# Performance work log

Hardware: AMD Instinct MI355X
Metric: run time of the kernel (lower is better)

The kernel has to match this reference:

```python
import jax, jax.numpy as jnp
import numpy as np

NODE_W, EDGE_W, HEADS = 512, 32, 8
DOT = NODE_W // HEADS
CLIP_MIN, CLIP_MAX = -5.0, 5.0
B, N = 4, 1024


def setup_inputs() -> dict:
    key = jax.random.key(0)
    ks = jax.random.split(key, 12)
    s = 0.02
    return {
        "nodes": jax.random.normal(ks[0], (B, N, NODE_W), dtype=jnp.float32),
        "edges": jax.random.normal(ks[1], (B, N, N, EDGE_W), dtype=jnp.float32),
        "Wq": jax.random.normal(ks[2], (NODE_W, NODE_W), dtype=jnp.float32) * s,
        "bq": jnp.zeros((NODE_W,), dtype=jnp.float32),
        "Wk": jax.random.normal(ks[3], (NODE_W, NODE_W), dtype=jnp.float32) * s,
        "bk": jnp.zeros((NODE_W,), dtype=jnp.float32),
        "Wv": jax.random.normal(ks[4], (NODE_W, NODE_W), dtype=jnp.float32) * s,
        "bv": jnp.zeros((NODE_W,), dtype=jnp.float32),
        "Wg": jax.random.normal(ks[5], (EDGE_W, HEADS), dtype=jnp.float32) * s,
        "bg": jnp.zeros((HEADS,), dtype=jnp.float32),
        "We": jax.random.normal(ks[6], (EDGE_W, HEADS), dtype=jnp.float32) * s,
        "be": jnp.zeros((HEADS,), dtype=jnp.float32),
    }


def reference(nodes, edges, Wq, bq, Wk, bk, Wv, bv, Wg, bg, We, be):
    b, n, _ = nodes.shape
    # projections, reshaped to [B, N, dot_dim, heads] as in the torch .view
    q = (nodes @ Wq + bq).reshape(b, n, DOT, HEADS)
    k = (nodes @ Wk + bk).reshape(b, n, DOT, HEADS)
    v = (nodes @ Wv + bv).reshape(b, n, DOT, HEADS)
    # raw scores [B, L, M, heads], scaled and clipped
    H = jnp.einsum('bldh,bmdh->blmh', q, k) / (DOT ** 0.5)
    H = jnp.clip(H, CLIP_MIN, CLIP_MAX)
    # edge bias and gate, each [B, N, N, heads]
    e = edges @ We + be
    g = edges @ Wg + bg
    H = H + e
    # softmax over key axis (dim=2), sigmoid gate multiply
    A = jax.nn.sigmoid(g) * jax.nn.softmax(H, axis=2)
    # dropout is identity in eval/deterministic mode
    attn = jnp.einsum('blmh,bmdh->bldh', A, v).reshape(b, n, NODE_W)
    return attn, H
```

## Files before the change

### kernel.cpp

```cpp
#include <hip/hip_runtime.h>
#include <hip/hip_bf16.h>
#include <stdint.h>

typedef float  f32x4  __attribute__((ext_vector_type(4)));
typedef short  bf16x8 __attribute__((ext_vector_type(8)));
typedef short  bf16x4 __attribute__((ext_vector_type(4)));

#define MFMA16(A,B,C) __builtin_amdgcn_mfma_f32_16x16x32_bf16(A,B,C,0,0,0)

__device__ __forceinline__ short f2bf(float x){
    union { float f; uint32_t u; } v; v.f = x;
    uint32_t r = v.u + 0x7fffu + ((v.u >> 16) & 1u);
    return (short)(r >> 16);
}
__device__ __forceinline__ float bf2f(short x){
    union { uint32_t u; float f; } v; v.u = ((uint32_t)(uint16_t)x) << 16;
    return v.f;
}
__device__ __forceinline__ bf16x8 pack8(f32x4 a, f32x4 b){
    bf16x8 r;
    r[0]=f2bf(a[0]); r[1]=f2bf(a[1]); r[2]=f2bf(a[2]); r[3]=f2bf(a[3]);
    r[4]=f2bf(b[0]); r[5]=f2bf(b[1]); r[6]=f2bf(b[2]); r[7]=f2bf(b[3]);
    return r;
}

__global__ void k_prep_wt(const float* __restrict__ Wq, const float* __restrict__ Wk,
                          const float* __restrict__ Wv, short* __restrict__ WT){
    int blk = blockIdx.x;
    int w  = blk >> 6;
    int t  = blk & 63;
    int k0 = (t >> 3) << 6;
    int o0 = (t & 7) << 6;
    const float* W = (w == 0) ? Wq : ((w == 1) ? Wk : Wv);
    __shared__ float tile[64][65];
    int tx = threadIdx.x & 63, ty = threadIdx.x >> 6;
    #pragma unroll
    for (int i = 0; i < 64; i += 4)
        tile[ty + i][tx] = W[(size_t)(k0 + ty + i) * 512 + o0 + tx];
    __syncthreads();
    short* out = WT + (size_t)w * 512 * 512;
    #pragma unroll
    for (int i = 0; i < 64; i += 4)
        out[(size_t)(o0 + ty + i) * 512 + k0 + tx] = f2bf(tile[tx][ty + i]);
}

__global__ void k_prep_wcat(const float* __restrict__ We, const float* __restrict__ Wg,
                            const float* __restrict__ be, const float* __restrict__ bg,
                            short* __restrict__ WcatT, float* __restrict__ bcat){
    int t = threadIdx.x;
    int ch = t >> 5, c = t & 31;
    float v = (ch < 8) ? We[c * 8 + ch] : Wg[c * 8 + (ch - 8)];
    WcatT[ch * 32 + c] = f2bf(v);
    if (t < 16) bcat[t] = (t < 8) ? be[t] : bg[t - 8];
}

__global__ void k_prep_nodes(const float* __restrict__ nodes, short* __restrict__ nb){
    size_t i = ((size_t)blockIdx.x * 256 + threadIdx.x) * 8;
    f32x4 a = *(const f32x4*)(nodes + i);
    f32x4 b = *(const f32x4*)(nodes + i + 4);
    *(bf16x8*)(nb + i) = pack8(a, b);
}

__global__ void k_qkv(const short* __restrict__ nodesbf, const short* __restrict__ WT,
                      const float* __restrict__ bq, const float* __restrict__ bk,
                      const float* __restrict__ bv,
                      short* __restrict__ qb, short* __restrict__ kb, short* __restrict__ vTb){
    int bx = blockIdx.x;
    int lt = bx & 255;
    int ob = bx >> 8;
    int wave = threadIdx.x >> 6, lane = threadIdx.x & 63;
    int lr = lane & 15, lg = lane >> 4;
    int row0 = lt << 4;
    int og = ob * 256 + wave * 64;
    int w  = og >> 9;
    int oo = og & 511;

    const short* Wp = WT + (size_t)w * 512 * 512;
    f32x4 acc[4] = {};
    const short* arow = nodesbf + (size_t)(row0 + lr) * 512 + lg * 8;
    #pragma unroll
    for (int kk = 0; kk < 16; ++kk){
        bf16x8 af = *(const bf16x8*)(arow + kk * 32);
        #pragma unroll
        for (int s = 0; s < 4; ++s){
            const short* bp = Wp + (size_t)(oo + s * 16 + lr) * 512 + kk * 32 + lg * 8;
            bf16x8 bfv = *(const bf16x8*)bp;
            acc[s] = MFMA16(af, bfv, acc[s]);
        }
    }
    const float* bias = (w == 0) ? bq : ((w == 1) ? bk : bv);
    int b  = row0 >> 10;
    int lb = (row0 & 1023) + lg * 4;
    #pragma unroll
    for (int s = 0; s < 4; ++s){
        int o = oo + s * 16 + lr;
        float bsv = bias[o];
        int h = o & 7, d = o >> 3;
        #pragma unroll
        for (int r = 0; r < 4; ++r){
            float v = acc[s][r] + bsv;
            short sv = f2bf(v);
            int l = lb + r;
            if (w == 0)       qb [((size_t)(b * 8 + h) * 1024 + l) * 64 + d] = sv;
            else if (w == 1)  kb [((size_t)(b * 8 + h) * 1024 + l) * 64 + d] = sv;
            else              vTb[((size_t)(b * 8 + h) * 64 + d) * 1024 + l] = sv;
        }
    }
}

__global__ void k_hsg(const float* __restrict__ edges, const short* __restrict__ qb,
                      const short* __restrict__ kb, const short* __restrict__ WcatT,
                      const float* __restrict__ bcat,
                      float* __restrict__ Hout, short* __restrict__ Pb,
                      float* __restrict__ psum){
    int bx = blockIdx.x;
    int mt = bx & 15;
    int lt = (bx >> 4) & 63;
    int b  = bx >> 10;
    int wave = threadIdx.x >> 6, lane = threadIdx.x & 63;
    int lr = lane & 15, lg = lane >> 4;
    int l0 = lt << 4;
    int m0 = mt * 64 + wave * 16;

    __shared__ short eg[4][16][16][24];

    f32x4 S[8] = {};
    #pragma unroll
    for (int h = 0; h < 8; ++h){
        #pragma unroll
        for (int half = 0; half < 2; ++half){
            bf16x8 qf = *(const bf16x8*)(qb + ((size_t)(b * 8 + h) * 1024 + l0 + lr) * 64 + half * 32 + lg * 8);
            bf16x8 kf = *(const bf16x8*)(kb + ((size_t)(b * 8 + h) * 1024 + m0 + lr) * 64 + half * 32 + lg * 8);
            S[h] = MFMA16(qf, kf, S[h]);
        }
    }

    bf16x8 wf = *(const bf16x8*)(WcatT + lr * 32 + lg * 8);
    f32x4 bc = *(const f32x4*)(bcat + lg * 4);
    f32x4 zero = {0.f, 0.f, 0.f, 0.f};
    #pragma unroll
    for (int l = 0; l < 16; ++l){
        const float* ep = edges + ((size_t)(b * 1024 + l0 + l) * 1024 + m0 + lr) * 32 + lg * 8;
        f32x4 e0 = *(const f32x4*)ep;
        f32x4 e1 = *(const f32x4*)(ep + 4);
        bf16x8 ef = pack8(e0, e1);
        f32x4 d = MFMA16(wf, ef, zero);
        bf16x4 dv;
        #pragma unroll
        for (int r = 0; r < 4; ++r) dv[r] = f2bf(d[r] + bc[r]);
        *(bf16x4*)&eg[wave][l][lr][lg * 4] = dv;
    }

    #pragma unroll
    for (int r = 0; r < 4; ++r){
        int l = lg * 4 + r;
        bf16x8 e8 = *(const bf16x8*)&eg[wave][l][lr][0];
        bf16x8 g8 = *(const bf16x8*)&eg[wave][l][lr][8];
        float Hv[8], ex[8], sg[8];
        #pragma unroll
        for (int h = 0; h < 8; ++h){
            float s = S[h][r] * 0.125f;
            s = fminf(fmaxf(s, -5.f), 5.f);
            Hv[h] = s + bf2f(e8[h]);
            ex[h] = __expf(Hv[h]);
            sg[h] = __builtin_amdgcn_rcpf(1.f + __expf(-bf2f(g8[h])));
        }
        size_t idx = ((size_t)(b * 1024 + l0 + l) * 1024 + m0 + lr) * 8;
        f32x4 h0 = {Hv[0], Hv[1], Hv[2], Hv[3]};
        f32x4 h1 = {Hv[4], Hv[5], Hv[6], Hv[7]};
        *(f32x4*)(Hout + idx)     = h0;
        *(f32x4*)(Hout + idx + 4) = h1;
        #pragma unroll
        for (int h = 0; h < 8; ++h){
            Pb[((size_t)(b * 8 + h) * 1024 + l0 + l) * 1024 + m0 + lr] = f2bf(ex[h] * sg[h]);
            float t = ex[h];
            t += __shfl_xor(t, 1);
            t += __shfl_xor(t, 2);
            t += __shfl_xor(t, 4);
            t += __shfl_xor(t, 8);
            if (lr == 0)
                psum[((size_t)(b * 8 + h) * 1024 + l0 + l) * 64 + mt * 4 + wave] = t;
        }
    }
}

__global__ void k_pv(const short* __restrict__ Pb, const float* __restrict__ psum,
                     const short* __restrict__ vTb, float* __restrict__ attn){
    int b  = blockIdx.x >> 6;
    int lt = blockIdx.x & 63;
    int h    = threadIdx.x >> 6;
    int lane = threadIdx.x & 63;
    int lr = lane & 15, lg = lane >> 4;
    int l0 = lt << 4;

    const short* Prow  = Pb  + ((size_t)(b * 8 + h) * 1024 + l0 + lr) * 1024 + lg * 8;
    const short* vbase = vTb + (size_t)(b * 8 + h) * 64 * 1024 + (size_t)lr * 1024 + lg * 8;

    f32x4 O[4] = {};
    for (int m0 = 0; m0 < 1024; m0 += 32){
        bf16x8 pf = *(const bf16x8*)(Prow + m0);
        #pragma unroll
        for (int dt = 0; dt < 4; ++dt){
            bf16x8 vf = *(const bf16x8*)(vbase + (size_t)dt * 16 * 1024 + m0);
            O[dt] = MFMA16(vf, pf, O[dt]);
        }
    }

    const float* pp = psum + ((size_t)(b * 8 + h) * 1024 + l0 + lr) * 64 + lg * 16;
    f32x4 s0 = *(const f32x4*)pp;
    f32x4 s1 = *(const f32x4*)(pp + 4);
    f32x4 s2 = *(const f32x4*)(pp + 8);
    f32x4 s3 = *(const f32x4*)(pp + 12);
    float ds = (s0[0]+s0[1]+s0[2]+s0[3]) + (s1[0]+s1[1]+s1[2]+s1[3])
             + (s2[0]+s2[1]+s2[2]+s2[3]) + (s3[0]+s3[1]+s3[2]+s3[3]);
    ds += __shfl_xor(ds, 16);
    ds += __shfl_xor(ds, 32);
    float inv = __builtin_amdgcn_rcpf(ds);

    __shared__ float Os[16][516];
    #pragma unroll
    for (int dt = 0; dt < 4; ++dt){
        #pragma unroll
        for (int r = 0; r < 4; ++r)
            Os[lr][(dt * 16 + lg * 4 + r) * 8 + h] = O[dt][r] * inv;
    }
    __syncthreads();
    int row = threadIdx.x >> 5;
    int cb  = (threadIdx.x & 31) * 16;
    float* dst = attn + ((size_t)(b * 1024 + l0 + row)) * 512 + cb;
    #pragma unroll
    for (int j = 0; j < 16; j += 4)
        *(f32x4*)(dst + j) = *(const f32x4*)&Os[row][cb + j];
}

#define OFF_WT    ((size_t)0x0000000)
#define OFF_WCAT  ((size_t)0x0180000)
#define OFF_BCAT  ((size_t)0x0180400)
#define OFF_NB    ((size_t)0x0200000)
#define OFF_Q     ((size_t)0x0600000)
#define OFF_K     ((size_t)0x0A00000)
#define OFF_VT    ((size_t)0x0E00000)
#define OFF_P     ((size_t)0x1200000)
#define OFF_PS    ((size_t)0x5200000)

extern "C" void kernel_launch(void* const* d_in, const int* in_sizes, int n_in,
                              void* d_out, int out_size, void* d_ws, size_t ws_size,
                              hipStream_t stream) {
    const float* nodes = (const float*)d_in[0];
    const float* edges = (const float*)d_in[1];
    const float* Wq = (const float*)d_in[2];
    const float* bq = (const float*)d_in[3];
    const float* Wk = (const float*)d_in[4];
    const float* bk = (const float*)d_in[5];
    const float* Wv = (const float*)d_in[6];
    const float* bv = (const float*)d_in[7];
    const float* Wg = (const float*)d_in[8];
    const float* bg = (const float*)d_in[9];
    const float* We = (const float*)d_in[10];
    const float* be = (const float*)d_in[11];

    float* out_attn = (float*)d_out;
    float* out_H    = out_attn + (size_t)4 * 1024 * 512;

    char* ws = (char*)d_ws;
    short* WT    = (short*)(ws + OFF_WT);
    short* WcatT = (short*)(ws + OFF_WCAT);
    float* bcat  = (float*)(ws + OFF_BCAT);
    short* nb    = (short*)(ws + OFF_NB);
    short* qb    = (short*)(ws + OFF_Q);
    short* kb    = (short*)(ws + OFF_K);
    short* vTb   = (short*)(ws + OFF_VT);
    short* Pb    = (short*)(ws + OFF_P);
    float* psum  = (float*)(ws + OFF_PS);

    k_prep_wt   <<<192, 256, 0, stream>>>(Wq, Wk, Wv, WT);
    k_prep_wcat <<<1, 512, 0, stream>>>(We, Wg, be, bg, WcatT, bcat);
    k_prep_nodes<<<1024, 256, 0, stream>>>(nodes, nb);
    k_qkv       <<<1536, 256, 0, stream>>>(nb, WT, bq, bk, bv, qb, kb, vTb);
    k_hsg       <<<4096, 256, 0, stream>>>(edges, qb, kb, WcatT, bcat, out_H, Pb, psum);
    k_pv        <<<256, 512, 0, stream>>>(Pb, psum, vTb, out_attn);
}
```

Before: 336.4 us.

## Fuse score/gate and PV kernels, keep probabilities in shared memory

Merges the score/edge-projection kernel and the P·V kernel into one kernel. Each block now owns 16 query rows and loops over all 1024 keys in chunks of 128. The gated probabilities are stored in a swizzled, double-buffered LDS tile and consumed right away by MFMA against V. The softmax denominators are accumulated in registers and reduced through LDS. This removes the global write and re-read of the bf16 P matrix and the partial-sum array, and edge loads are prefetched one step ahead in registers. In exchange the grid shrinks to 256 blocks of 512 threads with heavy register and LDS use, which lowers occupancy for an edges-bandwidth-bound stream.

After: 337.8 us. About the same (+0.4%).

```diff
diff --git a/kernel.cpp b/kernel.cpp
--- a/kernel.cpp
+++ b/kernel.cpp
@@ -108,129 +108,148 @@
     }
 }
 
-__global__ void k_hsg(const float* __restrict__ edges, const short* __restrict__ qb,
-                      const short* __restrict__ kb, const short* __restrict__ WcatT,
-                      const float* __restrict__ bcat,
-                      float* __restrict__ Hout, short* __restrict__ Pb,
-                      float* __restrict__ psum){
-    int bx = blockIdx.x;
-    int mt = bx & 15;
-    int lt = (bx >> 4) & 63;
-    int b  = bx >> 10;
-    int wave = threadIdx.x >> 6, lane = threadIdx.x & 63;
+__global__ __launch_bounds__(512, 2) void k_main(
+        const float* __restrict__ edges, const short* __restrict__ qb,
+        const short* __restrict__ kb, const short* __restrict__ vTb,
+        const short* __restrict__ WcatT, const float* __restrict__ bcat,
+        float* __restrict__ Hout, float* __restrict__ attn){
+    int hw = blockIdx.x;
+    int j  = hw & 7, kk0 = hw >> 3;
+    int b  = j >> 1;
+    int lt = ((j & 1) << 5) | kk0;
+    int l0 = lt << 4;
+
+    int w    = threadIdx.x >> 6;
+    int lane = threadIdx.x & 63;
     int lr = lane & 15, lg = lane >> 4;
-    int l0 = lt << 4;
-    int m0 = mt * 64 + wave * 16;
-
-    __shared__ short eg[4][16][16][24];
-
-    f32x4 S[8] = {};
+
+    __shared__ short eg[8][4][16][20];
+    __shared__ short Plds[2][8 * 16 * 128];
+    __shared__ float den[8][8][16];
+    __shared__ float Os[16][516];
+
+    bf16x8 wf = *(const bf16x8*)(WcatT + lr * 32 + lg * 8);
+    f32x4  bc = *(const f32x4*)(bcat + lg * 4);
+    const size_t bl0 = (size_t)(b * 1024 + l0);
+
+    f32x4 O[4] = {};
+    float dsum[8][4] = {};
+    f32x4 zero = {0.f, 0.f, 0.f, 0.f};
+
+    for (int iter = 0; iter < 8; ++iter){
+        const int m0 = iter * 128 + w * 16;
+        f32x4 S[8] = {};
+        #pragma unroll
+        for (int h = 0; h < 8; ++h){
+            #pragma unroll
+            for (int half = 0; half < 2; ++half){
+                bf16x8 qf = *(const bf16x8*)(qb + ((size_t)(b * 8 + h) * 1024 + l0 + lr) * 64 + half * 32 + lg * 8);
+                bf16x8 kf = *(const bf16x8*)(kb + ((size_t)(b * 8 + h) * 1024 + m0 + lr) * 64 + half * 32 + lg * 8);
+                S[h] = MFMA16(qf, kf, S[h]);
+            }
+        }
+
+        f32x4 ebuf[2][8];
+        #pragma unroll
+        for (int s = 0; s < 4; ++s){
+            const float* ep = edges + ((bl0 + 4 * s) * 1024 + m0 + lr) * 32 + lg * 8;
+            ebuf[0][2 * s]     = *(const f32x4*)ep;
+            ebuf[0][2 * s + 1] = *(const f32x4*)(ep + 4);
+        }
+        short* Pcur = &Plds[iter & 1][0];
+        #pragma unroll
+        for (int r = 0; r < 4; ++r){
+            if (r < 3){
+                #pragma unroll
+                for (int s = 0; s < 4; ++s){
+                    const float* ep = edges + ((bl0 + 4 * s + r + 1) * 1024 + m0 + lr) * 32 + lg * 8;
+                    ebuf[(r + 1) & 1][2 * s]     = *(const f32x4*)ep;
+                    ebuf[(r + 1) & 1][2 * s + 1] = *(const f32x4*)(ep + 4);
+                }
+            }
+            #pragma unroll
+            for (int s = 0; s < 4; ++s){
+                f32x4 d = MFMA16(wf, pack8(ebuf[r & 1][2 * s], ebuf[r & 1][2 * s + 1]), zero);
+                bf16x4 dv;
+                #pragma unroll
+                for (int rr = 0; rr < 4; ++rr) dv[rr] = f2bf(d[rr] + bc[rr]);
+                *(bf16x4*)&eg[w][s][lr][lg * 4] = dv;
+            }
+            int l = 4 * lg + r;
+            bf16x8 e8 = *(const bf16x8*)&eg[w][lg][lr][0];
+            bf16x8 g8 = *(const bf16x8*)&eg[w][lg][lr][8];
+            float Hv[8]; short pv[8];
+            #pragma unroll
+            for (int h = 0; h < 8; ++h){
+                float s = S[h][r] * 0.125f;
+                s = fminf(fmaxf(s, -5.f), 5.f);
+                float hv = s + bf2f(e8[h]);
+                Hv[h] = hv;
+                float ex = __expf(hv);
+                dsum[h][r] += ex;
+                float sg = __builtin_amdgcn_rcpf(1.f + __expf(-bf2f(g8[h])));
+                pv[h] = f2bf(ex * sg);
+            }
+            size_t idx = ((bl0 + l) * 1024 + m0 + lr) * 8;
+            f32x4 h0 = {Hv[0], Hv[1], Hv[2], Hv[3]};
+            f32x4 h1 = {Hv[4], Hv[5], Hv[6], Hv[7]};
+            *(f32x4*)(Hout + idx)     = h0;
+            *(f32x4*)(Hout + idx + 4) = h1;
+            #pragma unroll
+            for (int h = 0; h < 8; ++h){
+                int byte = ((h * 16 + l) << 8) + ((w * 16 + lr) << 1);
+                *(short*)((char*)Pcur + (byte ^ ((l & 7) << 4))) = pv[h];
+            }
+        }
+        __syncthreads();
+
+        const short* vbase = vTb + (size_t)(b * 8 + w) * 64 * 1024 + iter * 128;
+        #pragma unroll
+        for (int ks = 0; ks < 4; ++ks){
+            int mm = ks * 32 + lg * 8;
+            int byte = ((w * 16 + lr) << 8) + (mm << 1);
+            bf16x8 pf = *(const bf16x8*)((char*)Pcur + (byte ^ ((lr & 7) << 4)));
+            #pragma unroll
+            for (int dt = 0; dt < 4; ++dt){
+                bf16x8 vf = *(const bf16x8*)(vbase + (size_t)(dt * 16 + lr) * 1024 + mm);
+                O[dt] = MFMA16(vf, pf, O[dt]);
+            }
+        }
+    }
+
     #pragma unroll
     for (int h = 0; h < 8; ++h){
         #pragma unroll
-        for (int half = 0; half < 2; ++half){
-            bf16x8 qf = *(const bf16x8*)(qb + ((size_t)(b * 8 + h) * 1024 + l0 + lr) * 64 + half * 32 + lg * 8);
-            bf16x8 kf = *(const bf16x8*)(kb + ((size_t)(b * 8 + h) * 1024 + m0 + lr) * 64 + half * 32 + lg * 8);
-            S[h] = MFMA16(qf, kf, S[h]);
-        }
-    }
-
-    bf16x8 wf = *(const bf16x8*)(WcatT + lr * 32 + lg * 8);
-    f32x4 bc = *(const f32x4*)(bcat + lg * 4);
-    f32x4 zero = {0.f, 0.f, 0.f, 0.f};
-    #pragma unroll
-    for (int l = 0; l < 16; ++l){
-        const float* ep = edges + ((size_t)(b * 1024 + l0 + l) * 1024 + m0 + lr) * 32 + lg * 8;
-        f32x4 e0 = *(const f32x4*)ep;
-        f32x4 e1 = *(const f32x4*)(ep + 4);
-        bf16x8 ef = pack8(e0, e1);
-        f32x4 d = MFMA16(wf, ef, zero);
-        bf16x4 dv;
-        #pragma unroll
-        for (int r = 0; r < 4; ++r) dv[r] = f2bf(d[r] + bc[r]);
-        *(bf16x4*)&eg[wave][l][lr][lg * 4] = dv;
-    }
-
-    #pragma unroll
-    for (int r = 0; r < 4; ++r){
-        int l = lg * 4 + r;
-        bf16x8 e8 = *(const bf16x8*)&eg[wave][l][lr][0];
-        bf16x8 g8 = *(const bf16x8*)&eg[wave][l][lr][8];
-        float Hv[8], ex[8], sg[8];
-        #pragma unroll
-        for (int h = 0; h < 8; ++h){
-            float s = S[h][r] * 0.125f;
-            s = fminf(fmaxf(s, -5.f), 5.f);
-            Hv[h] = s + bf2f(e8[h]);
-            ex[h] = __expf(Hv[h]);
-            sg[h] = __builtin_amdgcn_rcpf(1.f + __expf(-bf2f(g8[h])));
-        }
-        size_t idx = ((size_t)(b * 1024 + l0 + l) * 1024 + m0 + lr) * 8;
-        f32x4 h0 = {Hv[0], Hv[1], Hv[2], Hv[3]};
-        f32x4 h1 = {Hv[4], Hv[5], Hv[6], Hv[7]};
-        *(f32x4*)(Hout + idx)     = h0;
-        *(f32x4*)(Hout + idx + 4) = h1;
-        #pragma unroll
-        for (int h = 0; h < 8; ++h){
-            Pb[((size_t)(b * 8 + h) * 1024 + l0 + l) * 1024 + m0 + lr] = f2bf(ex[h] * sg[h]);
-            float t = ex[h];
+        for (int r = 0; r < 4; ++r){
+            float t = dsum[h][r];
             t += __shfl_xor(t, 1);
             t += __shfl_xor(t, 2);
             t += __shfl_xor(t, 4);
             t += __shfl_xor(t, 8);
-            if (lr == 0)
-                psum[((size_t)(b * 8 + h) * 1024 + l0 + l) * 64 + mt * 4 + wave] = t;
-        }
-    }
-}
-
-__global__ void k_pv(const short* __restrict__ Pb, const float* __restrict__ psum,
-                     const short* __restrict__ vTb, float* __restrict__ attn){
-    int b  = blockIdx.x >> 6;
-    int lt = blockIdx.x & 63;
-    int h    = threadIdx.x >> 6;
-    int lane = threadIdx.x & 63;
-    int lr = lane & 15, lg = lane >> 4;
-    int l0 = lt << 4;
-
-    const short* Prow  = Pb  + ((size_t)(b * 8 + h) * 1024 + l0 + lr) * 1024 + lg * 8;
-    const short* vbase = vTb + (size_t)(b * 8 + h) * 64 * 1024 + (size_t)lr * 1024 + lg * 8;
-
-    f32x4 O[4] = {};
-    for (int m0 = 0; m0 < 1024; m0 += 32){
-        bf16x8 pf = *(const bf16x8*)(Prow + m0);
-        #pragma unroll
-        for (int dt = 0; dt < 4; ++dt){
-            bf16x8 vf = *(const bf16x8*)(vbase + (size_t)dt * 16 * 1024 + m0);
-            O[dt] = MFMA16(vf, pf, O[dt]);
-        }
-    }
-
-    const float* pp = psum + ((size_t)(b * 8 + h) * 1024 + l0 + lr) * 64 + lg * 16;
-    f32x4 s0 = *(const f32x4*)pp;
-    f32x4 s1 = *(const f32x4*)(pp + 4);
-    f32x4 s2 = *(const f32x4*)(pp + 8);
-    f32x4 s3 = *(const f32x4*)(pp + 12);
-    float ds = (s0[0]+s0[1]+s0[2]+s0[3]) + (s1[0]+s1[1]+s1[2]+s1[3])
-             + (s2[0]+s2[1]+s2[2]+s2[3]) + (s3[0]+s3[1]+s3[2]+s3[3]);
-    ds += __shfl_xor(ds, 16);
-    ds += __shfl_xor(ds, 32);
+            if (lr == 0) den[w][h][4 * lg + r] = t;
+        }
+    }
+    __syncthreads();
+    float ds = 0.f;
+    #pragma unroll
+    for (int w2 = 0; w2 < 8; ++w2) ds += den[w2][w][lr];
     float inv = __builtin_amdgcn_rcpf(ds);
 
-    __shared__ float Os[16][516];
     #pragma unroll
     for (int dt = 0; dt < 4; ++dt){
         #pragma unroll
         for (int r = 0; r < 4; ++r)
-            Os[lr][(dt * 16 + lg * 4 + r) * 8 + h] = O[dt][r] * inv;
+            Os[lr][(dt * 16 + 4 * lg + r) * 8 + w] = O[dt][r] * inv;
     }
     __syncthreads();
-    int row = threadIdx.x >> 5;
-    int cb  = (threadIdx.x & 31) * 16;
-    float* dst = attn + ((size_t)(b * 1024 + l0 + row)) * 512 + cb;
-    #pragma unroll
-    for (int j = 0; j < 16; j += 4)
-        *(f32x4*)(dst + j) = *(const f32x4*)&Os[row][cb + j];
+    {
+        int row = threadIdx.x >> 5;
+        int c0  = (threadIdx.x & 31) * 4;
+        float* dst = attn + (bl0 + row) * 512 + c0;
+        #pragma unroll
+        for (int jj = 0; jj < 4; ++jj)
+            *(f32x4*)(dst + jj * 128) = *(const f32x4*)&Os[row][c0 + jj * 128];
+    }
 }
 
 #define OFF_WT    ((size_t)0x0000000)
@@ -240,8 +259,6 @@
 #define OFF_Q     ((size_t)0x0600000)
 #define OFF_K     ((size_t)0x0A00000)
 #define OFF_VT    ((size_t)0x0E00000)
-#define OFF_P     ((size_t)0x1200000)
-#define OFF_PS    ((size_t)0x5200000)
 
 extern "C" void kernel_launch(void* const* d_in, const int* in_sizes, int n_in,
                               void* d_out, int out_size, void* d_ws, size_t ws_size,
@@ -270,13 +287,10 @@
     short* qb    = (short*)(ws + OFF_Q);
     short* kb    = (short*)(ws + OFF_K);
     short* vTb   = (short*)(ws + OFF_VT);
-    short* Pb    = (short*)(ws + OFF_P);
-    float* psum  = (float*)(ws + OFF_PS);
 
     k_prep_wt   <<<192, 256, 0, stream>>>(Wq, Wk, Wv, WT);
     k_prep_wcat <<<1, 512, 0, stream>>>(We, Wg, be, bg, WcatT, bcat);
     k_prep_nodes<<<1024, 256, 0, stream>>>(nodes, nb);
     k_qkv       <<<1536, 256, 0, stream>>>(nb, WT, bq, bk, bv, qb, kb, vTb);
-    k_hsg       <<<4096, 256, 0, stream>>>(edges, qb, kb, WcatT, bcat, out_H, Pb, psum);
-    k_pv        <<<256, 512, 0, stream>>>(Pb, psum, vTb, out_attn);
-}
+    k_main      <<<256, 512, 0, stream>>>(edges, qb, kb, vTb, WcatT, bcat, out_H, out_attn);
+}
```

## Stage QKV, H, P and row sums through LDS for coalesced tiled stores

Applied to the files above, without the earlier changes.

The QKV projection now transposes its output tile in shared memory and writes q/k/vT with 16-byte vector stores instead of scattered 2-byte stores. The fused score kernel stages H, P and the partial denominators in LDS so each is written as contiguous vectors, and P gets a tiled block layout that the PV kernel reads directly. Block indices are remapped so batches and row halves interleave, and launch bounds are added to the score kernel. The aim is to cut uncoalesced global write traffic, which dominates this memory-bound pipeline, at the cost of extra LDS usage and more complex indexing.

Result: faster. 293.8 us (-12.7%).

```diff
diff --git a/kernel.cpp b/kernel.cpp
--- a/kernel.cpp
+++ b/kernel.cpp
@@ -3,6 +3,7 @@
 #include <stdint.h>
 
 typedef float  f32x4  __attribute__((ext_vector_type(4)));
+typedef float  f32x2  __attribute__((ext_vector_type(2)));
 typedef short  bf16x8 __attribute__((ext_vector_type(8)));
 typedef short  bf16x4 __attribute__((ext_vector_type(4)));
 
@@ -74,6 +75,7 @@
     int og = ob * 256 + wave * 64;
     int w  = og >> 9;
     int oo = og & 511;
+    int dhalf = ob & 1;
 
     const short* Wp = WT + (size_t)w * 512 * 512;
     f32x4 acc[4] = {};
@@ -90,39 +92,61 @@
     }
     const float* bias = (w == 0) ? bq : ((w == 1) ? bk : bv);
     int b  = row0 >> 10;
-    int lb = (row0 & 1023) + lg * 4;
+    int lbase = row0 & 1023;
+
+    __shared__ short St[4096];
     #pragma unroll
     for (int s = 0; s < 4; ++s){
         int o = oo + s * 16 + lr;
         float bsv = bias[o];
-        int h = o & 7, d = o >> 3;
+        int h = o & 7, dd = (o >> 3) & 31;
         #pragma unroll
         for (int r = 0; r < 4; ++r){
-            float v = acc[s][r] + bsv;
-            short sv = f2bf(v);
-            int l = lb + r;
-            if (w == 0)       qb [((size_t)(b * 8 + h) * 1024 + l) * 64 + d] = sv;
-            else if (w == 1)  kb [((size_t)(b * 8 + h) * 1024 + l) * 64 + d] = sv;
-            else              vTb[((size_t)(b * 8 + h) * 64 + d) * 1024 + l] = sv;
-        }
-    }
-}
-
-__global__ void k_hsg(const float* __restrict__ edges, const short* __restrict__ qb,
-                      const short* __restrict__ kb, const short* __restrict__ WcatT,
-                      const float* __restrict__ bcat,
-                      float* __restrict__ Hout, short* __restrict__ Pb,
-                      float* __restrict__ psum){
+            short sv = f2bf(acc[s][r] + bsv);
+            int l = lg * 4 + r;
+            if (w < 2) St[(l << 8) + (h << 5) + dd] = sv;
+            else       St[(h << 9) + (dd << 4) + l] = sv;
+        }
+    }
+    __syncthreads();
+    int t = threadIdx.x;
+    bf16x8 v0 = *(const bf16x8*)&St[t * 16];
+    bf16x8 v1 = *(const bf16x8*)&St[t * 16 + 8];
+    if (w < 2){
+        short* dst = (w == 0) ? qb : kb;
+        int l = t >> 4, h = (t >> 1) & 7, dd0 = (t & 1) << 4;
+        size_t a = ((size_t)(b * 8 + h) * 1024 + lbase + l) * 64 + dhalf * 32 + dd0;
+        *(bf16x8*)(dst + a)     = v0;
+        *(bf16x8*)(dst + a + 8) = v1;
+    } else {
+        int h = t >> 5, dd = t & 31;
+        size_t a = ((size_t)(b * 8 + h) * 64 + dhalf * 32 + dd) * 1024 + lbase;
+        *(bf16x8*)(vTb + a)     = v0;
+        *(bf16x8*)(vTb + a + 8) = v1;
+    }
+}
+
+__global__ __launch_bounds__(256, 4) void k_hsg(
+        const float* __restrict__ edges, const short* __restrict__ qb,
+        const short* __restrict__ kb, const short* __restrict__ WcatT,
+        const float* __restrict__ bcat,
+        float* __restrict__ Hout, short* __restrict__ Pb,
+        float* __restrict__ psum){
     int bx = blockIdx.x;
-    int mt = bx & 15;
-    int lt = (bx >> 4) & 63;
-    int b  = bx >> 10;
-    int wave = threadIdx.x >> 6, lane = threadIdx.x & 63;
+    int j  = bx & 7;  int b = j >> 1;
+    int rest = bx >> 3;
+    int mt = rest & 15;
+    int lt = (rest >> 4) | ((j & 1) << 5);
+    int w = threadIdx.x >> 6, lane = threadIdx.x & 63;
     int lr = lane & 15, lg = lane >> 4;
     int l0 = lt << 4;
-    int m0 = mt * 64 + wave * 16;
-
-    __shared__ short eg[4][16][16][24];
+    int mg = (mt << 6) + (w << 4);
+    const size_t bl0 = (size_t)(b * 1024 + l0);
+
+    __shared__ short eg[4][4][16][24];
+    __shared__ float Hst[4][512];
+    __shared__ short Ps[4][2048];
+    __shared__ float den[4][128];
 
     f32x4 S[8] = {};
     #pragma unroll
@@ -130,89 +154,105 @@
         #pragma unroll
         for (int half = 0; half < 2; ++half){
             bf16x8 qf = *(const bf16x8*)(qb + ((size_t)(b * 8 + h) * 1024 + l0 + lr) * 64 + half * 32 + lg * 8);
-            bf16x8 kf = *(const bf16x8*)(kb + ((size_t)(b * 8 + h) * 1024 + m0 + lr) * 64 + half * 32 + lg * 8);
+            bf16x8 kf = *(const bf16x8*)(kb + ((size_t)(b * 8 + h) * 1024 + mg + lr) * 64 + half * 32 + lg * 8);
             S[h] = MFMA16(qf, kf, S[h]);
         }
     }
 
     bf16x8 wf = *(const bf16x8*)(WcatT + lr * 32 + lg * 8);
-    f32x4 bc = *(const f32x4*)(bcat + lg * 4);
+    f32x4  bc = *(const f32x4*)(bcat + lg * 4);
     f32x4 zero = {0.f, 0.f, 0.f, 0.f};
-    #pragma unroll
-    for (int l = 0; l < 16; ++l){
-        const float* ep = edges + ((size_t)(b * 1024 + l0 + l) * 1024 + m0 + lr) * 32 + lg * 8;
-        f32x4 e0 = *(const f32x4*)ep;
-        f32x4 e1 = *(const f32x4*)(ep + 4);
-        bf16x8 ef = pack8(e0, e1);
-        f32x4 d = MFMA16(wf, ef, zero);
-        bf16x4 dv;
-        #pragma unroll
-        for (int r = 0; r < 4; ++r) dv[r] = f2bf(d[r] + bc[r]);
-        *(bf16x4*)&eg[wave][l][lr][lg * 4] = dv;
-    }
 
     #pragma unroll
     for (int r = 0; r < 4; ++r){
-        int l = lg * 4 + r;
-        bf16x8 e8 = *(const bf16x8*)&eg[wave][l][lr][0];
-        bf16x8 g8 = *(const bf16x8*)&eg[wave][l][lr][8];
-        float Hv[8], ex[8], sg[8];
+        #pragma unroll
+        for (int s = 0; s < 4; ++s){
+            int l = 4 * s + r;
+            const float* ep = edges + ((bl0 + l) * 1024 + mg + lr) * 32 + lg * 8;
+            f32x4 e0 = *(const f32x4*)ep;
+            f32x4 e1 = *(const f32x4*)(ep + 4);
+            f32x4 d = MFMA16(wf, pack8(e0, e1), zero);
+            bf16x4 dv;
+            #pragma unroll
+            for (int rr = 0; rr < 4; ++rr) dv[rr] = f2bf(d[rr] + bc[rr]);
+            *(bf16x4*)&eg[w][s][lr][lg * 4] = dv;
+        }
+        int l = 4 * lg + r;
+        bf16x8 e8 = *(const bf16x8*)&eg[w][lg][lr][0];
+        bf16x8 g8 = *(const bf16x8*)&eg[w][lg][lr][8];
+        float Hv[8], ex[8];
         #pragma unroll
         for (int h = 0; h < 8; ++h){
             float s = S[h][r] * 0.125f;
             s = fminf(fmaxf(s, -5.f), 5.f);
             Hv[h] = s + bf2f(e8[h]);
             ex[h] = __expf(Hv[h]);
-            sg[h] = __builtin_amdgcn_rcpf(1.f + __expf(-bf2f(g8[h])));
-        }
-        size_t idx = ((size_t)(b * 1024 + l0 + l) * 1024 + m0 + lr) * 8;
-        f32x4 h0 = {Hv[0], Hv[1], Hv[2], Hv[3]};
-        f32x4 h1 = {Hv[4], Hv[5], Hv[6], Hv[7]};
-        *(f32x4*)(Hout + idx)     = h0;
-        *(f32x4*)(Hout + idx + 4) = h1;
+            float sg = __builtin_amdgcn_rcpf(1.f + __expf(-bf2f(g8[h])));
+            Ps[w][(h << 8) + (l << 4) + lr] = f2bf(ex[h] * sg);
+        }
         #pragma unroll
         for (int h = 0; h < 8; ++h){
-            Pb[((size_t)(b * 8 + h) * 1024 + l0 + l) * 1024 + m0 + lr] = f2bf(ex[h] * sg[h]);
             float t = ex[h];
             t += __shfl_xor(t, 1);
             t += __shfl_xor(t, 2);
             t += __shfl_xor(t, 4);
             t += __shfl_xor(t, 8);
-            if (lr == 0)
-                psum[((size_t)(b * 8 + h) * 1024 + l0 + l) * 64 + mt * 4 + wave] = t;
-        }
+            if (lr == 0) den[w][(h << 4) + l] = t;
+        }
+        f32x4 h0 = {Hv[0], Hv[1], Hv[2], Hv[3]};
+        f32x4 h1 = {Hv[4], Hv[5], Hv[6], Hv[7]};
+        *(f32x4*)&Hst[w][lg * 128 + lr * 8]     = h0;
+        *(f32x4*)&Hst[w][lg * 128 + lr * 8 + 4] = h1;
+        f32x4 o0 = *(const f32x4*)&Hst[w][lane * 4];
+        f32x4 o1 = *(const f32x4*)&Hst[w][256 + lane * 4];
+        int off = (lane * 4) & 127;
+        *(f32x4*)(Hout + (bl0 + 4 * (lane >> 5) + r)       * 8192 + mg * 8 + off) = o0;
+        *(f32x4*)(Hout + (bl0 + 4 * ((lane >> 5) + 2) + r) * 8192 + mg * 8 + off) = o1;
+    }
+
+    #pragma unroll
+    for (int jj = 0; jj < 4; ++jj){
+        int f = jj * 512 + lane * 8;
+        int h = f >> 8;
+        bf16x8 pv = *(const bf16x8*)&Ps[w][f];
+        size_t a = (((size_t)(b * 8 + h) * 64 + lt) * 64 + (mt * 4 + w)) * 256 + (f & 255);
+        *(bf16x8*)(Pb + a) = pv;
+    }
+    {
+        f32x2 dv = *(const f32x2*)&den[w][lane * 2];
+        size_t a = (((size_t)(b * 64 + lt) * 16 + mt) * 4 + w) * 128 + lane * 2;
+        *(f32x2*)(psum + a) = dv;
     }
 }
 
 __global__ void k_pv(const short* __restrict__ Pb, const float* __restrict__ psum,
                      const short* __restrict__ vTb, float* __restrict__ attn){
-    int b  = blockIdx.x >> 6;
-    int lt = blockIdx.x & 63;
+    int bx = blockIdx.x;
+    int j  = bx & 7;  int b = j >> 1;
+    int lt = ((j & 1) << 5) | (bx >> 3);
     int h    = threadIdx.x >> 6;
     int lane = threadIdx.x & 63;
     int lr = lane & 15, lg = lane >> 4;
     int l0 = lt << 4;
 
-    const short* Prow  = Pb  + ((size_t)(b * 8 + h) * 1024 + l0 + lr) * 1024 + lg * 8;
-    const short* vbase = vTb + (size_t)(b * 8 + h) * 64 * 1024 + (size_t)lr * 1024 + lg * 8;
+    const short* Pbase = Pb  + (((size_t)(b * 8 + h) * 64 + lt) * 64) * 256;
+    const short* vbase = vTb + (size_t)(b * 8 + h) * 65536;
 
     f32x4 O[4] = {};
-    for (int m0 = 0; m0 < 1024; m0 += 32){
-        bf16x8 pf = *(const bf16x8*)(Prow + m0);
+    for (int ks = 0; ks < 32; ++ks){
+        bf16x8 pf = *(const bf16x8*)(Pbase + (ks * 2 + (lg >> 1)) * 256 + lr * 16 + (lg & 1) * 8);
         #pragma unroll
         for (int dt = 0; dt < 4; ++dt){
-            bf16x8 vf = *(const bf16x8*)(vbase + (size_t)dt * 16 * 1024 + m0);
+            bf16x8 vf = *(const bf16x8*)(vbase + (size_t)(dt * 16 + lr) * 1024 + ks * 32 + lg * 8);
             O[dt] = MFMA16(vf, pf, O[dt]);
         }
     }
 
-    const float* pp = psum + ((size_t)(b * 8 + h) * 1024 + l0 + lr) * 64 + lg * 16;
-    f32x4 s0 = *(const f32x4*)pp;
-    f32x4 s1 = *(const f32x4*)(pp + 4);
-    f32x4 s2 = *(const f32x4*)(pp + 8);
-    f32x4 s3 = *(const f32x4*)(pp + 12);
-    float ds = (s0[0]+s0[1]+s0[2]+s0[3]) + (s1[0]+s1[1]+s1[2]+s1[3])
-             + (s2[0]+s2[1]+s2[2]+s2[3]) + (s3[0]+s3[1]+s3[2]+s3[3]);
+    const float* pp = psum + ((size_t)(b * 64 + lt) * 16) * 512;
+    float ds = 0.f;
+    #pragma unroll
+    for (int c = 0; c < 16; ++c)
+        ds += pp[(c * 4 + lg) * 128 + h * 16 + lr];
     ds += __shfl_xor(ds, 16);
     ds += __shfl_xor(ds, 32);
     float inv = __builtin_amdgcn_rcpf(ds);
@@ -229,8 +269,8 @@
     int cb  = (threadIdx.x & 31) * 16;
     float* dst = attn + ((size_t)(b * 1024 + l0 + row)) * 512 + cb;
     #pragma unroll
-    for (int j = 0; j < 16; j += 4)
-        *(f32x4*)(dst + j) = *(const f32x4*)&Os[row][cb + j];
+    for (int jj = 0; jj < 16; jj += 4)
+        *(f32x4*)(dst + jj) = *(const f32x4*)&Os[row][cb + jj];
 }
 
 #define OFF_WT    ((size_t)0x0000000)
```
